# Kernel tuning notes

Measured on AMD Instinct MI355X. Metric: run time of the kernel, lower is better.

Reference implementation:

```python
import jax, jax.numpy as jnp
import numpy as np

D_MODEL, D_K, D_V, D_H, SEQ = 1024, 64, 64, 16, 4096


def setup_inputs() -> dict:
    key = jax.random.key(0)
    ks = jax.random.split(key, 16)
    s = lambda fan_in: 1.0 / np.sqrt(fan_in)
    return {
        "X": jax.random.normal(ks[0], (SEQ, D_MODEL), jnp.float32),
        # shared Q/K/V projections (nn.Linear stores weight as [out, in])
        "Wq": jax.random.uniform(ks[1], (D_K, D_MODEL), jnp.float32, -s(D_MODEL), s(D_MODEL)),
        "bq": jax.random.uniform(ks[2], (D_K,), jnp.float32, -s(D_MODEL), s(D_MODEL)),
        "Wk": jax.random.uniform(ks[3], (D_K, D_MODEL), jnp.float32, -s(D_MODEL), s(D_MODEL)),
        "bk": jax.random.uniform(ks[4], (D_K,), jnp.float32, -s(D_MODEL), s(D_MODEL)),
        "Wv": jax.random.uniform(ks[5], (D_V, D_MODEL), jnp.float32, -s(D_MODEL), s(D_MODEL)),
        "bv": jax.random.uniform(ks[6], (D_V,), jnp.float32, -s(D_MODEL), s(D_MODEL)),
        # per-head linears stacked along head axis
        "Whq": jax.random.uniform(ks[7], (D_H, D_K, D_K), jnp.float32, -s(D_K), s(D_K)),
        "bhq": jax.random.uniform(ks[8], (D_H, D_K), jnp.float32, -s(D_K), s(D_K)),
        "Whk": jax.random.uniform(ks[9], (D_H, D_K, D_K), jnp.float32, -s(D_K), s(D_K)),
        "bhk": jax.random.uniform(ks[10], (D_H, D_K), jnp.float32, -s(D_K), s(D_K)),
        "Whv": jax.random.uniform(ks[11], (D_H, D_V, D_V), jnp.float32, -s(D_V), s(D_V)),
        "bhv": jax.random.uniform(ks[12], (D_H, D_V), jnp.float32, -s(D_V), s(D_V)),
        # final projection: d_h*d_v -> d_model
        "Wo": jax.random.uniform(ks[13], (D_MODEL, D_H * D_V), jnp.float32, -s(D_H * D_V), s(D_H * D_V)),
        "bo": jax.random.uniform(ks[14], (D_MODEL,), jnp.float32, -s(D_H * D_V), s(D_H * D_V)),
    }


def reference(X, Wq, bq, Wk, bk, Wv, bv, Whq, bhq, Whk, bhk, Whv, bhv, Wo, bo):
    # shared projections: [T, d_k] / [T, d_v]
    Q = X @ Wq.T + bq
    K = X @ Wk.T + bk
    V = X @ Wv.T + bv
    # per-head linears, all heads at once: [H, T, d_k]
    qh = jnp.einsum("tk,hjk->htj", Q, Whq) + bhq[:, None, :]
    kh = jnp.einsum("tk,hjk->htj", K, Whk) + bhk[:, None, :]
    vh = jnp.einsum("tv,hjv->htj", V, Whv) + bhv[:, None, :]
    # scaled dot-product attention per head: [H, T, T]
    scale = 1.0 / jnp.sqrt(jnp.asarray(Q.shape[-1], X.dtype))
    attn = jax.nn.softmax(jnp.einsum("htk,hsk->hts", qh, kh) * scale, axis=-1)
    rep = jnp.einsum("hts,hsv->htv", attn, vh)  # [H, T, d_v]
    # hstack heads -> [T, H*d_v], then final projection
    concat = rep.transpose(1, 0, 2).reshape(X.shape[0], -1)
    return concat @ Wo.T + bo
```

## Files before the change

kernel.cpp:

```cpp
#include <hip/hip_runtime.h>

#define T 4096
#define DM 1024
#define DK 64
#define H 16

typedef short s8 __attribute__((ext_vector_type(8)));
typedef float f4 __attribute__((ext_vector_type(4)));
typedef float f16v __attribute__((ext_vector_type(16)));
typedef unsigned short us4 __attribute__((ext_vector_type(4)));
typedef unsigned u32x2 __attribute__((ext_vector_type(2)));
typedef unsigned u32x4 __attribute__((ext_vector_type(4)));
typedef __bf16 bf2 __attribute__((ext_vector_type(2)));

#define MFMA16(a,b,c) __builtin_amdgcn_mfma_f32_16x16x32_bf16((a),(b),(c),0,0,0)
#define MFMA32(a,b,c) __builtin_amdgcn_mfma_f32_32x32x16_bf16((a),(b),(c),0,0,0)
#define SCALE_Q 0.18033688011112042f

__device__ __forceinline__ unsigned short f2bf(float x){
  __bf16 b = (__bf16)x;
  return __builtin_bit_cast(unsigned short, b);
}
__device__ __forceinline__ unsigned pk2(float a, float b){
  bf2 v; v[0] = (__bf16)a; v[1] = (__bf16)b;
  return __builtin_bit_cast(unsigned, v);
}

__device__ __forceinline__ void gload16(const void* g, void* lds){
  __builtin_amdgcn_global_load_lds((const __attribute__((address_space(1))) unsigned int*)g,
                                   (__attribute__((address_space(3))) unsigned int*)lds,
                                   16, 0, 0);
}

__device__ __forceinline__ void swp(unsigned X, unsigned Y, unsigned &E, unsigned &O){
#if __has_builtin(__builtin_amdgcn_permlane32_swap)
  auto a = __builtin_amdgcn_permlane32_swap(X, Y, false, false);
  E = a[0]; O = a[1];
#else
  int l = threadIdx.x & 63;
  unsigned sx = __builtin_amdgcn_ds_bpermute(((l & 31) << 2), X);
  unsigned sy = __builtin_amdgcn_ds_bpermute(((l & 31) << 2), Y);
  unsigned hx = __builtin_amdgcn_ds_bpermute((((l & 31) + 32) << 2), X);
  unsigned hy = __builtin_amdgcn_ds_bpermute((((l & 31) + 32) << 2), Y);
  E = (l < 32) ? sx : sy;
  O = (l < 32) ? hx : hy;
#endif
}

#define N_X   (T * DM / 4)
#define N_WOB (DM * DM / 4)
#define N_W3  (64 * DM / 4)
#define N_WH  (16 * 64 * 64 / 4)
__global__ __launch_bounds__(256) void prep_all(
    const float* __restrict__ X, const float* __restrict__ Wo,
    const float* __restrict__ Wq, const float* __restrict__ Wk, const float* __restrict__ Wv,
    const float* __restrict__ Whq, const float* __restrict__ Whk, const float* __restrict__ Whv,
    const float* __restrict__ bq, const float* __restrict__ bk, const float* __restrict__ bv,
    const float* __restrict__ bhq, const float* __restrict__ bhk, const float* __restrict__ bhv,
    unsigned short* __restrict__ Xbf, unsigned short* __restrict__ Wob,
    unsigned short* __restrict__ W3b, unsigned short* __restrict__ Whb,
    float* __restrict__ beff){
  int idx = blockIdx.x * 256 + threadIdx.x;
  if (idx < N_X){
    float4 v = reinterpret_cast<const float4*>(X)[idx];
    us4 o; o[0]=f2bf(v.x); o[1]=f2bf(v.y); o[2]=f2bf(v.z); o[3]=f2bf(v.w);
    reinterpret_cast<us4*>(Xbf)[idx] = o;
    return;
  }
  idx -= N_X;
  if (idx < N_WOB){
    float4 v = reinterpret_cast<const float4*>(Wo)[idx];
    us4 o; o[0]=f2bf(v.x); o[1]=f2bf(v.y); o[2]=f2bf(v.z); o[3]=f2bf(v.w);
    reinterpret_cast<us4*>(Wob)[idx] = o;
    return;
  }
  idx -= N_WOB;
  if (idx < 3 * N_W3){
    int seg = idx / N_W3, i = idx - seg * N_W3;
    const float* src = (seg == 0) ? Wq : ((seg == 1) ? Wk : Wv);
    float4 v = reinterpret_cast<const float4*>(src)[i];
    us4 o; o[0]=f2bf(v.x); o[1]=f2bf(v.y); o[2]=f2bf(v.z); o[3]=f2bf(v.w);
    reinterpret_cast<us4*>(W3b)[seg * N_W3 + i] = o;
    return;
  }
  idx -= 3 * N_W3;
  if (idx < 3 * N_WH){
    int seg = idx / N_WH, i = idx - seg * N_WH;
    const float* src = (seg == 0) ? Whq : ((seg == 1) ? Whk : Whv);
    float s = (seg == 0) ? SCALE_Q : 1.0f;
    float4 v = reinterpret_cast<const float4*>(src)[i];
    us4 o; o[0]=f2bf(v.x*s); o[1]=f2bf(v.y*s); o[2]=f2bf(v.z*s); o[3]=f2bf(v.w*s);
    reinterpret_cast<us4*>(Whb)[seg * N_WH + i] = o;
    return;
  }
  idx -= 3 * N_WH;
  if (idx < 3072){
    int seg = idx >> 10, j = idx & 1023;
    const float* Wh = (seg == 0) ? Whq : ((seg == 1) ? Whk : Whv);
    const float* b  = (seg == 0) ? bq  : ((seg == 1) ? bk  : bv);
    const float* bh = (seg == 0) ? bhq : ((seg == 1) ? bhk : bhv);
    float s = (seg == 0) ? SCALE_Q : 1.0f;
    const float* wr = Wh + j * 64;
    float acc = 0.f;
    #pragma unroll 8
    for (int k = 0; k < 64; ++k) acc += wr[k] * b[k];
    beff[idx] = (acc + bh[j]) * s;
  }
}

template<int MODE, int BM, int BN, int NT>
__global__ __launch_bounds__(256) void gemmX(const unsigned short* __restrict__ A,
                       const unsigned short* __restrict__ B,
                       const float* __restrict__ bias,
                       unsigned short* __restrict__ q_out,
                       unsigned short* __restrict__ k_out,
                       unsigned short* __restrict__ v_out,
                       float* __restrict__ f_out){
  __shared__ __align__(16) short la[2][BM * 64];
  __shared__ __align__(16) short lb[2][BN * 64];
  const int tid = threadIdx.x;
  const int wv = tid >> 6, l = tid & 63;
  const int lr = l & 15, lh = l >> 4;
  const int wr = wv >> 1, wc = wv & 1;
  const int tm = blockIdx.x / NT, tn = blockIdx.x % NT;
  const int t0 = tm * BM, o0 = tn * BN;
  constexpr int MF = BM / 32;
  constexpr int NF = BN / 32;
  constexpr int ACH = BM / 32;
  constexpr int BCH = BN / 32;
  constexpr int LAB = BM * 128;
  constexpr int LBB = BN * 128;

  f4 acc[MF][NF];
  #pragma unroll
  for (int i = 0; i < MF; ++i)
    #pragma unroll
    for (int j = 0; j < NF; ++j) acc[i][j] = (f4){0.f, 0.f, 0.f, 0.f};

  const int srow = tid >> 3;
  const int scs  = (tid & 7) ^ (srow & 7);
  const unsigned short* ap = A + (size_t)(t0 + srow) * DM + scs * 8;
  const unsigned short* bp = B + (size_t)(o0 + srow) * DM + scs * 8;
  char* ad = (char*)&la[0][0] + tid * 16;
  char* bd = (char*)&lb[0][0] + tid * 16;

  auto stage = [&](int BUF){
    #pragma unroll
    for (int i = 0; i < ACH; ++i)
      gload16(ap + (size_t)i * 32 * DM, ad + BUF * LAB + i * 4096);
    #pragma unroll
    for (int i = 0; i < BCH; ++i)
      gload16(bp + (size_t)i * 32 * DM, bd + BUF * LBB + i * 4096);
    ap += 64; bp += 64;
  };

  const int asw0 = (lh ^ (lr & 7)) * 16, asw1 = ((lh ^ 4) ^ (lr & 7)) * 16;
  const char* aB0 = (const char*)&la[0][0] + (wr * (BM / 2) + lr) * 128 + asw0;
  const char* aB1 = (const char*)&la[0][0] + (wr * (BM / 2) + lr) * 128 + asw1;
  const char* bB0 = (const char*)&lb[0][0] + (wc * (BN / 2) + lr) * 128 + asw0;
  const char* bB1 = (const char*)&lb[0][0] + (wc * (BN / 2) + lr) * 128 + asw1;

  auto step = [&](int BUF, bool dostage){
    if (dostage) stage(BUF ^ 1);
    s8 af[MF][2], bfr[NF][2];
    #pragma unroll
    for (int mf = 0; mf < MF; ++mf){
      af[mf][0] = *(const s8*)(aB0 + BUF * LAB + mf * 2048);
      af[mf][1] = *(const s8*)(aB1 + BUF * LAB + mf * 2048);
    }
    #pragma unroll
    for (int nf = 0; nf < NF; ++nf){
      bfr[nf][0] = *(const s8*)(bB0 + BUF * LBB + nf * 2048);
      bfr[nf][1] = *(const s8*)(bB1 + BUF * LBB + nf * 2048);
    }
    __builtin_amdgcn_s_setprio(1);
    #pragma unroll
    for (int mf = 0; mf < MF; ++mf)
      #pragma unroll
      for (int nf = 0; nf < NF; ++nf){
        acc[mf][nf] = MFMA16(af[mf][0], bfr[nf][0], acc[mf][nf]);
        acc[mf][nf] = MFMA16(af[mf][1], bfr[nf][1], acc[mf][nf]);
      }
    __builtin_amdgcn_s_setprio(0);
    __syncthreads();
  };

  stage(0);
  __syncthreads();
  #pragma unroll 1
  for (int t2 = 0; t2 < 8; ++t2){
    step(0, true);
    step(1, t2 < 7);
  }

  #pragma unroll
  for (int nf = 0; nf < NF; ++nf){
    int o = o0 + wc * (BN / 2) + nf * 16 + lr;
    float bs = (MODE == 4) ? 0.f : bias[o];
    int sel = o >> 6, oc = o & 63;
    unsigned short* yo = (sel == 0) ? q_out : ((sel == 1) ? k_out : v_out);
    #pragma unroll
    for (int mf = 0; mf < MF; ++mf)
      #pragma unroll
      for (int r = 0; r < 4; ++r){
        int t = t0 + wr * (BM / 2) + mf * 16 + lh * 4 + r;
        float v = acc[mf][nf][r] + bs;
        if (MODE == 2) f_out[(size_t)t * DM + o] = v;
        else           yo[(size_t)t * 64 + oc] = f2bf(v);
      }
  }
}

__global__ __launch_bounds__(256) void gemm_heads(const unsigned short* __restrict__ Yq,
                        const unsigned short* __restrict__ Yk,
                        const unsigned short* __restrict__ Yv,
                        const unsigned short* __restrict__ Whb,
                        const float* __restrict__ beff,
                        unsigned short* __restrict__ qhb,
                        unsigned short* __restrict__ khb,
                        unsigned short* __restrict__ vtb){
  const int tid = threadIdx.x;
  const int wv = tid >> 6, l = tid & 63;
  const int lr = l & 15, lh = l >> 4;
  const int rem = blockIdx.x % 48, tb = blockIdx.x / 48;
  const int kind = rem >> 4, h = rem & 15;
  const unsigned short* Y = (kind == 0) ? Yq : ((kind == 1) ? Yk : Yv);
  const unsigned short* B = Whb + (size_t)rem * 4096;
  const int t0 = tb * 256 + wv * 64;

  s8 wf[4][2], yf[4][2];
  #pragma unroll
  for (int nf = 0; nf < 4; ++nf)
    #pragma unroll
    for (int hf = 0; hf < 2; ++hf)
      wf[nf][hf] = *reinterpret_cast<const s8*>(B + (size_t)(nf * 16 + lr) * 64 + hf * 32 + lh * 8);
  #pragma unroll
  for (int mf = 0; mf < 4; ++mf)
    #pragma unroll
    for (int hf = 0; hf < 2; ++hf)
      yf[mf][hf] = *reinterpret_cast<const s8*>(Y + (size_t)(t0 + mf * 16 + lr) * 64 + hf * 32 + lh * 8);

  f4 acc[4][4];
  #pragma unroll
  for (int i = 0; i < 4; ++i)
    #pragma unroll
    for (int j = 0; j < 4; ++j) acc[i][j] = (f4){0.f, 0.f, 0.f, 0.f};

  if (kind < 2){
    #pragma unroll
    for (int mf = 0; mf < 4; ++mf)
      #pragma unroll
      for (int nf = 0; nf < 4; ++nf){
        acc[mf][nf] = MFMA16(yf[mf][0], wf[nf][0], acc[mf][nf]);
        acc[mf][nf] = MFMA16(yf[mf][1], wf[nf][1], acc[mf][nf]);
      }
    unsigned short* out = (kind == 0) ? qhb : khb;
    #pragma unroll
    for (int nf = 0; nf < 4; ++nf){
      int j = nf * 16 + lr;
      float bs = beff[rem * 64 + j];
      #pragma unroll
      for (int mf = 0; mf < 4; ++mf)
        #pragma unroll
        for (int r = 0; r < 4; ++r){
          int t = t0 + mf * 16 + lh * 4 + r;
          out[((size_t)h * T + t) * DK + j] = f2bf(acc[mf][nf][r] + bs);
        }
    }
  } else {
    #pragma unroll
    for (int nf = 0; nf < 4; ++nf)
      #pragma unroll
      for (int mf = 0; mf < 4; ++mf){
        acc[nf][mf] = MFMA16(wf[nf][0], yf[mf][0], acc[nf][mf]);
        acc[nf][mf] = MFMA16(wf[nf][1], yf[mf][1], acc[nf][mf]);
      }
    #pragma unroll
    for (int nf = 0; nf < 4; ++nf){
      float4 bsv = *reinterpret_cast<const float4*>(beff + rem * 64 + nf * 16 + lh * 4);
      #pragma unroll
      for (int r = 0; r < 4; ++r){
        int j = nf * 16 + lh * 4 + r;
        float bs = (r == 0) ? bsv.x : ((r == 1) ? bsv.y : ((r == 2) ? bsv.z : bsv.w));
        #pragma unroll
        for (int mf = 0; mf < 4; ++mf){
          int t = t0 + mf * 16 + lr;
          vtb[((size_t)h * DK + j) * T + t] = f2bf(acc[nf][mf][r] + bs);
        }
      }
    }
  }
}

__global__ __launch_bounds__(256) void attn_fwd(const unsigned short* __restrict__ qh,
                         const unsigned short* __restrict__ kh,
                         const unsigned short* __restrict__ vt,
                         unsigned short* __restrict__ cat){
  __shared__ __align__(16) char ldsb[2][32768];
  const int tid = threadIdx.x;
  const int wv = tid >> 6, l = tid & 63;
  const int l31 = l & 31, h5 = l >> 5, l7 = l & 7;
  const int h = blockIdx.x >> 5, qblk = blockIdx.x & 31;
  const int Q0w = qblk * 128 + wv * 32;

  s8 qf[4];
  #pragma unroll
  for (int kk = 0; kk < 4; ++kk)
    qf[kk] = *reinterpret_cast<const s8*>(
        qh + ((size_t)h * T + Q0w + l31) * DK + kk * 16 + h5 * 8);

  float ls = 0.f;
  f16v oa0, oa1;
  #pragma unroll
  for (int i = 0; i < 16; ++i){ oa0[i] = 0.f; oa1[i] = 0.f; }

  const int srow = tid >> 3;
  const int scs  = (tid & 7) ^ (srow & 7);
  const unsigned short* kp = kh + (size_t)h * T * DK + srow * DK + scs * 8;
  const unsigned short* vp = vt + (size_t)h * DK * T + srow * T + scs * 8;
  char* sd = &ldsb[0][0] + tid * 16;

  auto stage = [&](int BUF){
    const int b = BUF * 32768;
    gload16(kp,            sd + b);
    gload16(kp + 32 * DK,  sd + b + 4096);
    gload16(vp,            sd + b + 8192);
    gload16(vp + 32 * T,   sd + b + 12288);
    gload16(kp + 64 * DK,  sd + b + 16384);
    gload16(kp + 96 * DK,  sd + b + 20480);
    gload16(vp + 64,       sd + b + 24576);
    gload16(vp + 32 * T + 64, sd + b + 28672);
    kp += 128 * DK; vp += 128;
  };

  const char* ba[2][4];
  #pragma unroll
  for (int t2 = 0; t2 < 2; ++t2)
    #pragma unroll
    for (int kk = 0; kk < 4; ++kk)
      ba[t2][kk] = &ldsb[0][0] + (t2 * 32 + l31) * 128 + ((((kk << 1) | h5) ^ l7) << 4);

  auto subtile = [&](int boff){
    s8 kf0[4], kf1[4];
    #pragma unroll
    for (int kk = 0; kk < 4; ++kk){
      kf0[kk] = *(const s8*)(ba[0][kk] + boff);
      kf1[kk] = *(const s8*)(ba[1][kk] + boff);
    }
    f16v sc0, sc1;
    #pragma unroll
    for (int i = 0; i < 16; ++i){ sc0[i] = 0.f; sc1[i] = 0.f; }
    __builtin_amdgcn_s_setprio(1);
    #pragma unroll
    for (int kk = 0; kk < 4; ++kk) sc0 = MFMA32(kf0[kk], qf[kk], sc0);
    #pragma unroll
    for (int kk = 0; kk < 4; ++kk) sc1 = MFMA32(kf1[kk], qf[kk], sc1);
    __builtin_amdgcn_s_setprio(0);
    s8 vf0[4], vf1[4];
    #pragma unroll
    for (int p = 0; p < 4; ++p){
      vf0[p] = *(const s8*)(ba[0][p] + boff + 8192);
      vf1[p] = *(const s8*)(ba[1][p] + boff + 8192);
    }
    float p0[16], p1[16];
    #pragma unroll
    for (int i = 0; i < 16; ++i){
      p0[i] = __builtin_amdgcn_exp2f(sc0[i]);
      p1[i] = __builtin_amdgcn_exp2f(sc1[i]);
    }
    float r0 = (p0[0]+p0[1]) + (p0[2]+p0[3]);
    float r1 = (p0[4]+p0[5]) + (p0[6]+p0[7]);
    float r2 = (p0[8]+p0[9]) + (p0[10]+p0[11]);
    float r3 = (p0[12]+p0[13]) + (p0[14]+p0[15]);
    float r4 = (p1[0]+p1[1]) + (p1[2]+p1[3]);
    float r5 = (p1[4]+p1[5]) + (p1[6]+p1[7]);
    float r6 = (p1[8]+p1[9]) + (p1[10]+p1[11]);
    float r7 = (p1[12]+p1[13]) + (p1[14]+p1[15]);
    ls += ((r0+r1)+(r2+r3)) + ((r4+r5)+(r6+r7));
    unsigned a0 = pk2(p0[0],p0[1]),  a1 = pk2(p0[2],p0[3]);
    unsigned a2 = pk2(p0[4],p0[5]),  a3 = pk2(p0[6],p0[7]);
    unsigned a4 = pk2(p0[8],p0[9]),  a5 = pk2(p0[10],p0[11]);
    unsigned a6 = pk2(p0[12],p0[13]), a7 = pk2(p0[14],p0[15]);
    unsigned b0 = pk2(p1[0],p1[1]),  b1 = pk2(p1[2],p1[3]);
    unsigned b2 = pk2(p1[4],p1[5]),  b3 = pk2(p1[6],p1[7]);
    unsigned b4 = pk2(p1[8],p1[9]),  b5 = pk2(p1[10],p1[11]);
    unsigned b6 = pk2(p1[12],p1[13]), b7 = pk2(p1[14],p1[15]);
    unsigned e0,o0, e1,o1, e2,o2, e3,o3, e4,o4, e5,o5, e6,o6, e7,o7;
    swp(a0, a2, e0, o0);  swp(a1, a3, e1, o1);
    swp(a4, a6, e2, o2);  swp(a5, a7, e3, o3);
    swp(b0, b2, e4, o4);  swp(b1, b3, e5, o5);
    swp(b4, b6, e6, o6);  swp(b5, b7, e7, o7);
    u32x4 pu0 = {e0, e1, o0, o1};
    u32x4 pu1 = {e2, e3, o2, o3};
    u32x4 pu2 = {e4, e5, o4, o5};
    u32x4 pu3 = {e6, e7, o6, o7};
    s8 pa0 = __builtin_bit_cast(s8, pu0);
    s8 pa1 = __builtin_bit_cast(s8, pu1);
    s8 pa2 = __builtin_bit_cast(s8, pu2);
    s8 pa3 = __builtin_bit_cast(s8, pu3);
    __builtin_amdgcn_s_setprio(1);
    oa0 = MFMA32(vf0[0], pa0, oa0);
    oa0 = MFMA32(vf0[1], pa1, oa0);
    oa0 = MFMA32(vf0[2], pa2, oa0);
    oa0 = MFMA32(vf0[3], pa3, oa0);
    oa1 = MFMA32(vf1[0], pa0, oa1);
    oa1 = MFMA32(vf1[1], pa1, oa1);
    oa1 = MFMA32(vf1[2], pa2, oa1);
    oa1 = MFMA32(vf1[3], pa3, oa1);
    __builtin_amdgcn_s_setprio(0);
  };

  stage(0);
  __syncthreads();
  #pragma unroll 1
  for (int it = 0; it < 32; ++it){
    const int BUF = it & 1;
    if (it < 31) stage(BUF ^ 1);
    subtile(BUF * 32768);
    subtile(BUF * 32768 + 16384);
    __syncthreads();
  }

  float lq = ls + __shfl_xor(ls, 32);
  float inv = 1.f / lq;
  const int t = Q0w + l31;
  unsigned short* crow = cat + (size_t)t * DM + h * DK;
  #pragma unroll
  for (int g = 0; g < 4; ++g){
    u32x2 w0, w1;
    w0[0] = pk2(oa0[g*4+0] * inv, oa0[g*4+1] * inv);
    w0[1] = pk2(oa0[g*4+2] * inv, oa0[g*4+3] * inv);
    w1[0] = pk2(oa1[g*4+0] * inv, oa1[g*4+1] * inv);
    w1[1] = pk2(oa1[g*4+2] * inv, oa1[g*4+3] * inv);
    *reinterpret_cast<u32x2*>(crow + g * 8 + h5 * 4)      = w0;
    *reinterpret_cast<u32x2*>(crow + 32 + g * 8 + h5 * 4) = w1;
  }
}

extern "C" void kernel_launch(void* const* d_in, const int* in_sizes, int n_in,
                              void* d_out, int out_size, void* d_ws, size_t ws_size,
                              hipStream_t stream){
  const float* X   = (const float*)d_in[0];
  const float* Wq  = (const float*)d_in[1];
  const float* bq  = (const float*)d_in[2];
  const float* Wk  = (const float*)d_in[3];
  const float* bk  = (const float*)d_in[4];
  const float* Wv  = (const float*)d_in[5];
  const float* bv  = (const float*)d_in[6];
  const float* Whq = (const float*)d_in[7];
  const float* bhq = (const float*)d_in[8];
  const float* Whk = (const float*)d_in[9];
  const float* bhk = (const float*)d_in[10];
  const float* Whv = (const float*)d_in[11];
  const float* bhv = (const float*)d_in[12];
  const float* Wo  = (const float*)d_in[13];
  const float* bo  = (const float*)d_in[14];

  char* w = (char*)d_ws;
  size_t off = 0;
  auto alloc = [&](size_t bytes) -> char* {
    char* p = w + off;
    off = (off + bytes + 255) & ~(size_t)255;
    return p;
  };
  unsigned short* Xbf = (unsigned short*)alloc((size_t)T * DM * 2);
  unsigned short* Wob = (unsigned short*)alloc((size_t)DM * DM * 2);
  unsigned short* W3b = (unsigned short*)alloc((size_t)192 * DM * 2);
  unsigned short* Whb = (unsigned short*)alloc((size_t)48 * 64 * 64 * 2);
  float* beff = (float*)alloc(48 * 64 * 4);
  unsigned short* Yq  = (unsigned short*)alloc((size_t)T * 64 * 2);
  unsigned short* Yk  = (unsigned short*)alloc((size_t)T * 64 * 2);
  unsigned short* Yv  = (unsigned short*)alloc((size_t)T * 64 * 2);
  unsigned short* qhb = (unsigned short*)alloc((size_t)H * T * DK * 2);
  unsigned short* khb = (unsigned short*)alloc((size_t)H * T * DK * 2);
  unsigned short* vtb = (unsigned short*)alloc((size_t)H * T * DK * 2);
  unsigned short* cat = Xbf;

  {
    int total = N_X + N_WOB + 3 * N_W3 + 3 * N_WH + 3072;
    prep_all<<<(total + 255) / 256, 256, 0, stream>>>(
        X, Wo, Wq, Wk, Wv, Whq, Whk, Whv, bq, bk, bv, bhq, bhk, bhv,
        Xbf, Wob, W3b, Whb, beff);
  }

  gemmX<4, 64, 64, 3><<<(T / 64) * 3, 256, 0, stream>>>(Xbf, W3b, nullptr, Yq, Yk, Yv, nullptr);

  gemm_heads<<<(T / 256) * 48, 256, 0, stream>>>(Yq, Yk, Yv, Whb, beff, qhb, khb, vtb);

  attn_fwd<<<(T / 128) * H, 256, 0, stream>>>(qhb, khb, vtb, cat);

  gemmX<2, 128, 64, 16><<<(T / 128) * 16, 256, 0, stream>>>(cat, Wob, bo, nullptr, nullptr, nullptr, (float*)d_out);
}
```

Baseline: 142.9 us.

## Give each wave private K/V staging buffers and drop block-wide barriers

The attention kernel now stages K and V tiles into per-wave LDS buffers of 32 keys each, double-buffered, so each wave streams its own copy of the keys. Synchronization uses explicit vmcnt and lgkmcnt waits instead of __syncthreads, and the next load is issued as soon as the current buffer has been read into registers. This removes the cross-wave barrier stalls and allows deeper per-wave prefetch. The cost is four times the global and L2 traffic for K/V, since every wave loads the same tiles, plus smaller MFMA batches per iteration.

New measurement: 166.1 us. 16.3% more time.

```diff
diff --git a/kernel.cpp b/kernel.cpp
--- a/kernel.cpp
+++ b/kernel.cpp
@@ -296,7 +296,7 @@
                          const unsigned short* __restrict__ kh,
                          const unsigned short* __restrict__ vt,
                          unsigned short* __restrict__ cat){
-  __shared__ __align__(16) char ldsb[2][32768];
+  __shared__ __align__(16) char ldsb[4][2][8192];
   const int tid = threadIdx.x;
   const int wv = tid >> 6, l = tid & 63;
   const int l31 = l & 31, h5 = l >> 5, l7 = l & 7;
@@ -314,111 +314,94 @@
   #pragma unroll
   for (int i = 0; i < 16; ++i){ oa0[i] = 0.f; oa1[i] = 0.f; }
 
-  const int srow = tid >> 3;
-  const int scs  = (tid & 7) ^ (srow & 7);
-  const unsigned short* kp = kh + (size_t)h * T * DK + srow * DK + scs * 8;
-  const unsigned short* vp = vt + (size_t)h * DK * T + srow * T + scs * 8;
-  char* sd = &ldsb[0][0] + tid * 16;
+  const int krow = l >> 3;
+  const int kcs  = (l & 7) ^ (krow & 7);
+  const unsigned short* kp = kh + (size_t)h * T * DK + krow * DK + kcs * 8;
+  const int vrow = l >> 2;
+  const int vcs  = (l & 3) ^ (vrow & 3);
+  const unsigned short* vp = vt + (size_t)h * DK * T + vrow * T + vcs * 8;
+  char* kd = &ldsb[wv][0][0] + l * 16;
+  char* vd = &ldsb[wv][0][0] + 4096 + l * 16;
 
   auto stage = [&](int BUF){
-    const int b = BUF * 32768;
-    gload16(kp,            sd + b);
-    gload16(kp + 32 * DK,  sd + b + 4096);
-    gload16(vp,            sd + b + 8192);
-    gload16(vp + 32 * T,   sd + b + 12288);
-    gload16(kp + 64 * DK,  sd + b + 16384);
-    gload16(kp + 96 * DK,  sd + b + 20480);
-    gload16(vp + 64,       sd + b + 24576);
-    gload16(vp + 32 * T + 64, sd + b + 28672);
-    kp += 128 * DK; vp += 128;
+    const int b = BUF * 8192;
+    gload16(kp,            kd + b);
+    gload16(kp + 8 * DK,   kd + b + 1024);
+    gload16(kp + 16 * DK,  kd + b + 2048);
+    gload16(kp + 24 * DK,  kd + b + 3072);
+    gload16(vp,            vd + b);
+    gload16(vp + 16 * T,   vd + b + 1024);
+    gload16(vp + 32 * T,   vd + b + 2048);
+    gload16(vp + 48 * T,   vd + b + 3072);
+    kp += 32 * DK; vp += 32;
   };
 
-  const char* ba[2][4];
-  #pragma unroll
-  for (int t2 = 0; t2 < 2; ++t2)
-    #pragma unroll
-    for (int kk = 0; kk < 4; ++kk)
-      ba[t2][kk] = &ldsb[0][0] + (t2 * 32 + l31) * 128 + ((((kk << 1) | h5) ^ l7) << 4);
-
-  auto subtile = [&](int boff){
-    s8 kf0[4], kf1[4];
-    #pragma unroll
-    for (int kk = 0; kk < 4; ++kk){
-      kf0[kk] = *(const s8*)(ba[0][kk] + boff);
-      kf1[kk] = *(const s8*)(ba[1][kk] + boff);
-    }
-    f16v sc0, sc1;
-    #pragma unroll
-    for (int i = 0; i < 16; ++i){ sc0[i] = 0.f; sc1[i] = 0.f; }
+  const char* kb[4];
+  #pragma unroll
+  for (int kk = 0; kk < 4; ++kk)
+    kb[kk] = &ldsb[wv][0][0] + l31 * 128 + ((((kk << 1) | h5) ^ l7) << 4);
+  const char* vb[2][2];
+  #pragma unroll
+  for (int dt = 0; dt < 2; ++dt)
+    #pragma unroll
+    for (int ks = 0; ks < 2; ++ks)
+      vb[dt][ks] = &ldsb[wv][0][0] + 4096 + (dt * 32 + l31) * 64 +
+                   ((((ks << 1) | h5) ^ (l31 & 3)) << 4);
+
+  stage(0);
+  stage(1);
+
+  #pragma unroll 1
+  for (int it = 0; it < 128; ++it){
+    const int BUF = it & 1;
+    if (it < 127) asm volatile("s_waitcnt vmcnt(8)" ::: "memory");
+    else          asm volatile("s_waitcnt vmcnt(0)" ::: "memory");
+    __builtin_amdgcn_sched_barrier(0);
+
+    const int bo = BUF * 8192;
+    s8 kf[4], vf[2][2];
+    #pragma unroll
+    for (int kk = 0; kk < 4; ++kk) kf[kk] = *(const s8*)(kb[kk] + bo);
+    #pragma unroll
+    for (int dt = 0; dt < 2; ++dt)
+      #pragma unroll
+      for (int ks = 0; ks < 2; ++ks) vf[dt][ks] = *(const s8*)(vb[dt][ks] + bo);
+    asm volatile("s_waitcnt lgkmcnt(0)" ::: "memory");
+    __builtin_amdgcn_sched_barrier(0);
+    if (it < 126) stage(BUF);
+
+    f16v sc;
+    #pragma unroll
+    for (int i = 0; i < 16; ++i) sc[i] = 0.f;
     __builtin_amdgcn_s_setprio(1);
     #pragma unroll
-    for (int kk = 0; kk < 4; ++kk) sc0 = MFMA32(kf0[kk], qf[kk], sc0);
-    #pragma unroll
-    for (int kk = 0; kk < 4; ++kk) sc1 = MFMA32(kf1[kk], qf[kk], sc1);
+    for (int kk = 0; kk < 4; ++kk) sc = MFMA32(kf[kk], qf[kk], sc);
     __builtin_amdgcn_s_setprio(0);
-    s8 vf0[4], vf1[4];
-    #pragma unroll
-    for (int p = 0; p < 4; ++p){
-      vf0[p] = *(const s8*)(ba[0][p] + boff + 8192);
-      vf1[p] = *(const s8*)(ba[1][p] + boff + 8192);
-    }
-    float p0[16], p1[16];
-    #pragma unroll
-    for (int i = 0; i < 16; ++i){
-      p0[i] = __builtin_amdgcn_exp2f(sc0[i]);
-      p1[i] = __builtin_amdgcn_exp2f(sc1[i]);
-    }
-    float r0 = (p0[0]+p0[1]) + (p0[2]+p0[3]);
-    float r1 = (p0[4]+p0[5]) + (p0[6]+p0[7]);
-    float r2 = (p0[8]+p0[9]) + (p0[10]+p0[11]);
-    float r3 = (p0[12]+p0[13]) + (p0[14]+p0[15]);
-    float r4 = (p1[0]+p1[1]) + (p1[2]+p1[3]);
-    float r5 = (p1[4]+p1[5]) + (p1[6]+p1[7]);
-    float r6 = (p1[8]+p1[9]) + (p1[10]+p1[11]);
-    float r7 = (p1[12]+p1[13]) + (p1[14]+p1[15]);
-    ls += ((r0+r1)+(r2+r3)) + ((r4+r5)+(r6+r7));
-    unsigned a0 = pk2(p0[0],p0[1]),  a1 = pk2(p0[2],p0[3]);
-    unsigned a2 = pk2(p0[4],p0[5]),  a3 = pk2(p0[6],p0[7]);
-    unsigned a4 = pk2(p0[8],p0[9]),  a5 = pk2(p0[10],p0[11]);
-    unsigned a6 = pk2(p0[12],p0[13]), a7 = pk2(p0[14],p0[15]);
-    unsigned b0 = pk2(p1[0],p1[1]),  b1 = pk2(p1[2],p1[3]);
-    unsigned b2 = pk2(p1[4],p1[5]),  b3 = pk2(p1[6],p1[7]);
-    unsigned b4 = pk2(p1[8],p1[9]),  b5 = pk2(p1[10],p1[11]);
-    unsigned b6 = pk2(p1[12],p1[13]), b7 = pk2(p1[14],p1[15]);
-    unsigned e0,o0, e1,o1, e2,o2, e3,o3, e4,o4, e5,o5, e6,o6, e7,o7;
+    float p[16];
+    #pragma unroll
+    for (int i = 0; i < 16; ++i) p[i] = __builtin_amdgcn_exp2f(sc[i]);
+    float r0 = (p[0]+p[1]) + (p[2]+p[3]);
+    float r1 = (p[4]+p[5]) + (p[6]+p[7]);
+    float r2 = (p[8]+p[9]) + (p[10]+p[11]);
+    float r3 = (p[12]+p[13]) + (p[14]+p[15]);
+    ls += (r0+r1) + (r2+r3);
+    unsigned a0 = pk2(p[0],p[1]),  a1 = pk2(p[2],p[3]);
+    unsigned a2 = pk2(p[4],p[5]),  a3 = pk2(p[6],p[7]);
+    unsigned a4 = pk2(p[8],p[9]),  a5 = pk2(p[10],p[11]);
+    unsigned a6 = pk2(p[12],p[13]), a7 = pk2(p[14],p[15]);
+    unsigned e0,o0, e1,o1, e2,o2, e3,o3;
     swp(a0, a2, e0, o0);  swp(a1, a3, e1, o1);
     swp(a4, a6, e2, o2);  swp(a5, a7, e3, o3);
-    swp(b0, b2, e4, o4);  swp(b1, b3, e5, o5);
-    swp(b4, b6, e6, o6);  swp(b5, b7, e7, o7);
     u32x4 pu0 = {e0, e1, o0, o1};
     u32x4 pu1 = {e2, e3, o2, o3};
-    u32x4 pu2 = {e4, e5, o4, o5};
-    u32x4 pu3 = {e6, e7, o6, o7};
     s8 pa0 = __builtin_bit_cast(s8, pu0);
     s8 pa1 = __builtin_bit_cast(s8, pu1);
-    s8 pa2 = __builtin_bit_cast(s8, pu2);
-    s8 pa3 = __builtin_bit_cast(s8, pu3);
     __builtin_amdgcn_s_setprio(1);
-    oa0 = MFMA32(vf0[0], pa0, oa0);
-    oa0 = MFMA32(vf0[1], pa1, oa0);
-    oa0 = MFMA32(vf0[2], pa2, oa0);
-    oa0 = MFMA32(vf0[3], pa3, oa0);
-    oa1 = MFMA32(vf1[0], pa0, oa1);
-    oa1 = MFMA32(vf1[1], pa1, oa1);
-    oa1 = MFMA32(vf1[2], pa2, oa1);
-    oa1 = MFMA32(vf1[3], pa3, oa1);
+    oa0 = MFMA32(vf[0][0], pa0, oa0);
+    oa0 = MFMA32(vf[0][1], pa1, oa0);
+    oa1 = MFMA32(vf[1][0], pa0, oa1);
+    oa1 = MFMA32(vf[1][1], pa1, oa1);
     __builtin_amdgcn_s_setprio(0);
-  };
-
-  stage(0);
-  __syncthreads();
-  #pragma unroll 1
-  for (int it = 0; it < 32; ++it){
-    const int BUF = it & 1;
-    if (it < 31) stage(BUF ^ 1);
-    subtile(BUF * 32768);
-    subtile(BUF * 32768 + 16384);
-    __syncthreads();
   }
 
   float lq = ls + __shfl_xor(ls, 32);
```
